# Performance work log

Hardware: AMD Instinct MI355X
Metric: run time of the kernel (lower is better)

## Reference

```python
import jax, jax.numpy as jnp
import numpy as np


def setup_inputs() -> dict:
    key = jax.random.key(0)
    ks = jax.random.split(key, 5)
    B, T, D, U = 32, 2048, 512, 512
    scale = 1.0 / np.sqrt(D)
    return {
        "full": jax.random.normal(ks[0], (B, T, D), jnp.float32),
        "last": jax.random.normal(ks[1], (B, D), jnp.float32),
        "W1": jax.random.normal(ks[2], (D, U), jnp.float32) * scale,
        "b1": jnp.zeros((U,), jnp.float32),
        "W2": jax.random.normal(ks[3], (D, U), jnp.float32) * scale,
        "b2": jnp.zeros((U,), jnp.float32),
        "V": jax.random.normal(ks[4], (U, 1), jnp.float32) * (1.0 / np.sqrt(U)),
        "bV": jnp.zeros((1,), jnp.float32),
    }


def reference(full, last, W1, b1, W2, b2, V, bV):
    # full: [B,T,D], last: [B,D]
    h1 = jnp.einsum("btd,du->btu", full, W1) + b1          # [B,T,U]
    h2 = last @ W2 + b2                                      # [B,U]
    score = jnp.tanh(h1 + h2[:, None, :]) @ V + bV           # [B,T,1]
    attn = jax.nn.softmax(score, axis=1)                     # [B,T,1]
    context = jnp.sum(attn * full, axis=1)                   # [B,D]
    return context
```

## Files before the change

### kernel.cpp

```cpp
#include <hip/hip_runtime.h>
#include <math.h>


#define BB 32
#define TT 2048
#define DD 512
#define UU 512

typedef short bf16x8 __attribute__((ext_vector_type(8)));
typedef short bf16x4 __attribute__((ext_vector_type(4)));
typedef float f32x4  __attribute__((ext_vector_type(4)));

static __device__ __forceinline__ short f2bf(float f) {
    unsigned x = __float_as_uint(f);
    return (short)((x + 0x7fffu + ((x >> 16) & 1u)) >> 16);
}

static __device__ __forceinline__ float fast_tanh(float x) {
    float e = __expf(2.f * x);
    return 1.f - 2.f * __builtin_amdgcn_rcpf(e + 1.f);
}

__global__ __launch_bounds__(256) void prep_kernel(const float* __restrict__ W1,
                                                   short* __restrict__ W1T,
                                                   const float* __restrict__ last,
                                                   const float* __restrict__ W2,
                                                   const float* __restrict__ b1,
                                                   const float* __restrict__ b2,
                                                   float* __restrict__ h2) {
    __shared__ float tile[32][33];
    __shared__ float ls[DD];
    const int bid = blockIdx.x;
    const int tid = threadIdx.x;
    if (bid < 256) {
        const int tr = (bid >> 4) << 5;
        const int tc = (bid & 15) << 5;
#pragma unroll
        for (int p = 0; p < 4; ++p) {
            const int r = p * 8 + (tid >> 5), c = tid & 31;
            tile[r][c] = W1[(size_t)(tr + r) * UU + tc + c];
        }
        __syncthreads();
#pragma unroll
        for (int p = 0; p < 4; ++p) {
            const int r = p * 8 + (tid >> 5), c = tid & 31;
            W1T[(size_t)(tc + r) * DD + tr + c] = f2bf(tile[c][r]);
        }
    } else {
        const int b = bid - 256;
        for (int i = tid; i < DD; i += 256) ls[i] = last[b * DD + i];
        __syncthreads();
        float a0 = 0.f, a1 = 0.f;
#pragma unroll 8
        for (int d = 0; d < DD; ++d) {
            const float l = ls[d];
            a0 += l * W2[d * UU + tid];
            a1 += l * W2[d * UU + tid + 256];
        }
        h2[b * UU + tid]       = a0 + b1[tid] + b2[tid];
        h2[b * UU + tid + 256] = a1 + b1[tid + 256] + b2[tid + 256];
    }
}

__global__ __launch_bounds__(256, 2) void score_kernel(const float* __restrict__ full,
                                                       const short* __restrict__ W1T,
                                                       const float* __restrict__ h2,
                                                       const float* __restrict__ V,
                                                       float* __restrict__ scores) {
    __shared__ __align__(16) short a_lds[64 * 40];
    __shared__ __align__(16) short b_lds[512 * 32];
    __shared__ float h2s[UU];
    __shared__ float Vs[UU];
    __shared__ float score_red[64];

    const int bid = blockIdx.x;
    const int b  = bid >> 5;
    const int t0 = (bid & 31) << 6;
    const int tid = threadIdx.x;
    const int w    = tid >> 6;
    const int lane = tid & 63;
    const int quad = lane >> 4;
    const int col  = lane & 15;

    for (int i = tid; i < UU; i += 256) { h2s[i] = h2[b * UU + i]; Vs[i] = V[i]; }
    if (tid < 64) score_red[tid] = 0.f;

    f32x4 acc[4][8];
#pragma unroll
    for (int i = 0; i < 4; ++i)
#pragma unroll
        for (int j = 0; j < 8; ++j) acc[i][j] = (f32x4){0.f, 0.f, 0.f, 0.f};

    const int arow = tid >> 3;
    const int ac   = (tid & 7) << 2;

    for (int k0 = 0; k0 < DD; k0 += 32) {
#pragma unroll
        for (int i = 0; i < 2; ++i) {
            const int row = arow + 32 * i;
            const float4 v = *(const float4*)&full[((size_t)(b * TT + t0 + row)) * DD + k0 + ac];
            bf16x4 s = {f2bf(v.x), f2bf(v.y), f2bf(v.z), f2bf(v.w)};
            *(bf16x4*)&a_lds[row * 40 + ac] = s;
        }
#pragma unroll
        for (int i = 0; i < 8; ++i) {
            const int id = (w * 8 + i) * 64 + lane;
            const int u  = id >> 2;
            const int c  = (id & 3) ^ (u & 3);
            const short* g = W1T + (size_t)u * DD + k0 + c * 8;
            __builtin_amdgcn_global_load_lds(
                (const __attribute__((address_space(1))) void*)g,
                (__attribute__((address_space(3))) void*)&b_lds[(w * 8 + i) * 64 * 8],
                16, 0, 0);
        }
        __syncthreads();

        bf16x8 af[4];
#pragma unroll
        for (int mt = 0; mt < 4; ++mt)
            af[mt] = *(const bf16x8*)&a_lds[(mt * 16 + col) * 40 + quad * 8];
#pragma unroll
        for (int nt = 0; nt < 8; ++nt) {
            const int u = w * 128 + nt * 16 + col;
            const bf16x8 bf = *(const bf16x8*)&b_lds[(u * 4 + (quad ^ (u & 3))) * 8];
#pragma unroll
            for (int mt = 0; mt < 4; ++mt)
                acc[mt][nt] = __builtin_amdgcn_mfma_f32_16x16x32_bf16(af[mt], bf, acc[mt][nt], 0, 0, 0);
        }
        __syncthreads();
    }

    float srow[16];
#pragma unroll
    for (int i = 0; i < 16; ++i) srow[i] = 0.f;
#pragma unroll
    for (int mt = 0; mt < 4; ++mt) {
#pragma unroll
        for (int nt = 0; nt < 8; ++nt) {
            const int u = w * 128 + nt * 16 + col;
            const float hv = h2s[u];
            const float vv = Vs[u];
#pragma unroll
            for (int r = 0; r < 4; ++r)
                srow[mt * 4 + r] += fast_tanh(acc[mt][nt][r] + hv) * vv;
        }
    }
#pragma unroll
    for (int off = 1; off < 16; off <<= 1) {
#pragma unroll
        for (int i = 0; i < 16; ++i) srow[i] += __shfl_xor(srow[i], off, 64);
    }
    if (col == 0) {
#pragma unroll
        for (int mt = 0; mt < 4; ++mt)
#pragma unroll
            for (int r = 0; r < 4; ++r)
                atomicAdd(&score_red[mt * 16 + quad * 4 + r], srow[mt * 4 + r]);
    }
    __syncthreads();
    if (tid < 64) scores[b * TT + t0 + tid] = score_red[tid];
}

__global__ __launch_bounds__(256) void softmax_kernel(float* __restrict__ scores,
                                                      float* __restrict__ out) {
    const int b = blockIdx.x;
    const int tid = threadIdx.x;
    __shared__ float red[256];

    out[b * DD + tid] = 0.f;
    out[b * DD + 256 + tid] = 0.f;

    float local[8];
    float m = -1e30f;
#pragma unroll
    for (int i = 0; i < 8; ++i) {
        local[i] = scores[b * TT + i * 256 + tid];
        m = fmaxf(m, local[i]);
    }
    red[tid] = m;
    __syncthreads();
    for (int s = 128; s > 0; s >>= 1) {
        if (tid < s) red[tid] = fmaxf(red[tid], red[tid + s]);
        __syncthreads();
    }
    const float mx = red[0];
    __syncthreads();

    float sum = 0.f;
#pragma unroll
    for (int i = 0; i < 8; ++i) {
        local[i] = __expf(local[i] - mx);
        sum += local[i];
    }
    red[tid] = sum;
    __syncthreads();
    for (int s = 128; s > 0; s >>= 1) {
        if (tid < s) red[tid] += red[tid + s];
        __syncthreads();
    }
    const float inv = 1.f / red[0];
#pragma unroll
    for (int i = 0; i < 8; ++i) scores[b * TT + i * 256 + tid] = local[i] * inv;
}

__global__ __launch_bounds__(256) void context_kernel(const float* __restrict__ full,
                                                      const float* __restrict__ p,
                                                      float* __restrict__ out) {
    const int bid = blockIdx.x;
    const int b  = bid >> 5;
    const int t0 = (bid & 31) << 6;
    const int tid = threadIdx.x;
    const int q   = tid & 127;
    const int par = tid >> 7;
    __shared__ float ps[64];
    __shared__ float4 red[128];
    if (tid < 64) ps[tid] = p[b * TT + t0 + tid];
    __syncthreads();

    float ax = 0.f, ay = 0.f, az = 0.f, aw = 0.f;
    const float* base = full + ((size_t)(b * TT + t0)) * DD;
#pragma unroll 4
    for (int it = 0; it < 32; ++it) {
        const int tl = it * 2 + par;
        const float4 v = *(const float4*)&base[(size_t)tl * DD + q * 4];
        const float wg = ps[tl];
        ax += wg * v.x; ay += wg * v.y; az += wg * v.z; aw += wg * v.w;
    }
    if (par == 1) red[q] = make_float4(ax, ay, az, aw);
    __syncthreads();
    if (par == 0) {
        const float4 o = red[q];
        atomicAdd(&out[b * DD + q * 4 + 0], ax + o.x);
        atomicAdd(&out[b * DD + q * 4 + 1], ay + o.y);
        atomicAdd(&out[b * DD + q * 4 + 2], az + o.z);
        atomicAdd(&out[b * DD + q * 4 + 3], aw + o.w);
    }
}

extern "C" void kernel_launch(void* const* d_in, const int* in_sizes, int n_in,
                              void* d_out, int out_size, void* d_ws, size_t ws_size,
                              hipStream_t stream) {
    const float* full = (const float*)d_in[0];
    const float* last = (const float*)d_in[1];
    const float* W1   = (const float*)d_in[2];
    const float* b1   = (const float*)d_in[3];
    const float* W2   = (const float*)d_in[4];
    const float* b2   = (const float*)d_in[5];
    const float* V    = (const float*)d_in[6];

    float* out    = (float*)d_out;
    float* scores = (float*)d_ws;
    float* h2     = (float*)d_ws + (size_t)BB * TT;
    short* W1T    = (short*)(h2 + (size_t)BB * UU);

    prep_kernel<<<256 + BB, 256, 0, stream>>>(W1, W1T, last, W2, b1, b2, h2);
    score_kernel<<<BB * (TT / 64), 256, 0, stream>>>(full, W1T, h2, V, scores);
    softmax_kernel<<<BB, 256, 0, stream>>>(scores, out);
    context_kernel<<<BB * (TT / 64), 256, 0, stream>>>(full, scores, out);
}
```

Baseline: 302.3 us.

## Load W1 fragments from global directly and restage A tiles with swizzled LDS

```diff
diff --git a/kernel.cpp b/kernel.cpp
--- a/kernel.cpp
+++ b/kernel.cpp
@@ -8,7 +8,6 @@
 #define UU 512
 
 typedef short bf16x8 __attribute__((ext_vector_type(8)));
-typedef short bf16x4 __attribute__((ext_vector_type(4)));
 typedef float f32x4  __attribute__((ext_vector_type(4)));
 
 static __device__ __forceinline__ short f2bf(float f) {
@@ -67,11 +66,8 @@
                                                        const float* __restrict__ h2,
                                                        const float* __restrict__ V,
                                                        float* __restrict__ scores) {
-    __shared__ __align__(16) short a_lds[64 * 40];
-    __shared__ __align__(16) short b_lds[512 * 32];
-    __shared__ float h2s[UU];
-    __shared__ float Vs[UU];
-    __shared__ float score_red[64];
+    __shared__ __align__(16) short a_lds[1024 * 8];
+    __shared__ float score_red[4][64];
 
     const int bid = blockIdx.x;
     const int b  = bid >> 5;
@@ -82,68 +78,63 @@
     const int quad = lane >> 4;
     const int col  = lane & 15;
 
-    for (int i = tid; i < UU; i += 256) { h2s[i] = h2[b * UU + i]; Vs[i] = V[i]; }
-    if (tid < 64) score_red[tid] = 0.f;
-
     f32x4 acc[4][8];
 #pragma unroll
     for (int i = 0; i < 4; ++i)
 #pragma unroll
         for (int j = 0; j < 8; ++j) acc[i][j] = (f32x4){0.f, 0.f, 0.f, 0.f};
 
-    const int arow = tid >> 3;
-    const int ac   = (tid & 7) << 2;
-
-    for (int k0 = 0; k0 < DD; k0 += 32) {
-#pragma unroll
-        for (int i = 0; i < 2; ++i) {
-            const int row = arow + 32 * i;
-            const float4 v = *(const float4*)&full[((size_t)(b * TT + t0 + row)) * DD + k0 + ac];
-            bf16x4 s = {f2bf(v.x), f2bf(v.y), f2bf(v.z), f2bf(v.w)};
-            *(bf16x4*)&a_lds[row * 40 + ac] = s;
-        }
-#pragma unroll
-        for (int i = 0; i < 8; ++i) {
-            const int id = (w * 8 + i) * 64 + lane;
-            const int u  = id >> 2;
-            const int c  = (id & 3) ^ (u & 3);
-            const short* g = W1T + (size_t)u * DD + k0 + c * 8;
-            __builtin_amdgcn_global_load_lds(
-                (const __attribute__((address_space(1))) void*)g,
-                (__attribute__((address_space(3))) void*)&b_lds[(w * 8 + i) * 64 * 8],
-                16, 0, 0);
-        }
-        __syncthreads();
-
-        bf16x8 af[4];
+    const size_t fullbase = (size_t)(b * TT + t0) * DD;
+    const short* bbase = W1T + (size_t)(w * 128 + col) * DD + quad * 8;
+
+    for (int ko = 0; ko < 4; ++ko) {
+        if (ko > 0) __syncthreads();
+#pragma unroll
+        for (int i = 0; i < 4; ++i) {
+            const int id  = tid + 256 * i;
+            const int row = id >> 4;
+            const int cc  = (id & 15) ^ (row & 15);
+            const float* src = &full[fullbase + (size_t)row * DD + ko * 128 + cc * 8];
+            const float4 v0 = *(const float4*)src;
+            const float4 v1 = *(const float4*)(src + 4);
+            bf16x8 pk = {f2bf(v0.x), f2bf(v0.y), f2bf(v0.z), f2bf(v0.w),
+                         f2bf(v1.x), f2bf(v1.y), f2bf(v1.z), f2bf(v1.w)};
+            *(bf16x8*)&a_lds[id * 8] = pk;
+        }
+        __syncthreads();
+
+        for (int ki = 0; ki < 4; ++ki) {
+            bf16x8 af[4];
+#pragma unroll
+            for (int mt = 0; mt < 4; ++mt) {
+                const int row = mt * 16 + col;
+                const int sl  = row * 16 + ((ki * 4 + quad) ^ col);
+                af[mt] = *(const bf16x8*)&a_lds[sl * 8];
+            }
+            const int kg = ko * 128 + ki * 32;
+#pragma unroll
+            for (int nt = 0; nt < 8; ++nt) {
+                const bf16x8 bf = *(const bf16x8*)&bbase[(size_t)nt * 16 * DD + kg];
+#pragma unroll
+                for (int mt = 0; mt < 4; ++mt)
+                    acc[mt][nt] = __builtin_amdgcn_mfma_f32_16x16x32_bf16(af[mt], bf, acc[mt][nt], 0, 0, 0);
+            }
+        }
+    }
+
+    float srow[16];
+#pragma unroll
+    for (int i = 0; i < 16; ++i) srow[i] = 0.f;
+#pragma unroll
+    for (int nt = 0; nt < 8; ++nt) {
+        const int u = w * 128 + nt * 16 + col;
+        const float hv = h2[b * UU + u];
+        const float vv = V[u];
 #pragma unroll
         for (int mt = 0; mt < 4; ++mt)
-            af[mt] = *(const bf16x8*)&a_lds[(mt * 16 + col) * 40 + quad * 8];
-#pragma unroll
-        for (int nt = 0; nt < 8; ++nt) {
-            const int u = w * 128 + nt * 16 + col;
-            const bf16x8 bf = *(const bf16x8*)&b_lds[(u * 4 + (quad ^ (u & 3))) * 8];
-#pragma unroll
-            for (int mt = 0; mt < 4; ++mt)
-                acc[mt][nt] = __builtin_amdgcn_mfma_f32_16x16x32_bf16(af[mt], bf, acc[mt][nt], 0, 0, 0);
-        }
-        __syncthreads();
-    }
-
-    float srow[16];
-#pragma unroll
-    for (int i = 0; i < 16; ++i) srow[i] = 0.f;
-#pragma unroll
-    for (int mt = 0; mt < 4; ++mt) {
-#pragma unroll
-        for (int nt = 0; nt < 8; ++nt) {
-            const int u = w * 128 + nt * 16 + col;
-            const float hv = h2s[u];
-            const float vv = Vs[u];
 #pragma unroll
             for (int r = 0; r < 4; ++r)
                 srow[mt * 4 + r] += fast_tanh(acc[mt][nt][r] + hv) * vv;
-        }
     }
 #pragma unroll
     for (int off = 1; off < 16; off <<= 1) {
@@ -155,10 +146,12 @@
         for (int mt = 0; mt < 4; ++mt)
 #pragma unroll
             for (int r = 0; r < 4; ++r)
-                atomicAdd(&score_red[mt * 16 + quad * 4 + r], srow[mt * 4 + r]);
-    }
-    __syncthreads();
-    if (tid < 64) scores[b * TT + t0 + tid] = score_red[tid];
+                score_red[w][mt * 16 + quad * 4 + r] = srow[mt * 4 + r];
+    }
+    __syncthreads();
+    if (tid < 64)
+        scores[b * TT + t0 + tid] = score_red[0][tid] + score_red[1][tid] +
+                                    score_red[2][tid] + score_red[3][tid];
 }
 
 __global__ __launch_bounds__(256) void softmax_kernel(float* __restrict__ scores,
@@ -207,33 +200,40 @@
                                                       const float* __restrict__ p,
                                                       float* __restrict__ out) {
     const int bid = blockIdx.x;
-    const int b  = bid >> 5;
-    const int t0 = (bid & 31) << 6;
-    const int tid = threadIdx.x;
-    const int q   = tid & 127;
-    const int par = tid >> 7;
-    __shared__ float ps[64];
-    __shared__ float4 red[128];
-    if (tid < 64) ps[tid] = p[b * TT + t0 + tid];
+    const int b  = bid >> 3;
+    const int d0 = ((bid >> 1) & 3) * 128;
+    const int t0 = (bid & 1) * 1024;
+    const int tid = threadIdx.x;
+    const int c  = tid & 31;
+    const int tr = tid >> 5;
+
+    __shared__ float ps[1024];
+    __shared__ float4 red[256];
+    for (int i = tid; i < 1024; i += 256) ps[i] = p[b * TT + t0 + i];
     __syncthreads();
 
     float ax = 0.f, ay = 0.f, az = 0.f, aw = 0.f;
-    const float* base = full + ((size_t)(b * TT + t0)) * DD;
+    const float* base = full + ((size_t)(b * TT + t0)) * DD + d0;
 #pragma unroll 4
-    for (int it = 0; it < 32; ++it) {
-        const int tl = it * 2 + par;
-        const float4 v = *(const float4*)&base[(size_t)tl * DD + q * 4];
-        const float wg = ps[tl];
+    for (int it = 0; it < 128; ++it) {
+        const int t = it * 8 + tr;
+        const float4 v = *(const float4*)&base[(size_t)t * DD + c * 4];
+        const float wg = ps[t];
         ax += wg * v.x; ay += wg * v.y; az += wg * v.z; aw += wg * v.w;
     }
-    if (par == 1) red[q] = make_float4(ax, ay, az, aw);
-    __syncthreads();
-    if (par == 0) {
-        const float4 o = red[q];
-        atomicAdd(&out[b * DD + q * 4 + 0], ax + o.x);
-        atomicAdd(&out[b * DD + q * 4 + 1], ay + o.y);
-        atomicAdd(&out[b * DD + q * 4 + 2], az + o.z);
-        atomicAdd(&out[b * DD + q * 4 + 3], aw + o.w);
+    red[tid] = make_float4(ax, ay, az, aw);
+    __syncthreads();
+    if (tid < 32) {
+        float4 s = red[tid];
+#pragma unroll
+        for (int g = 1; g < 8; ++g) {
+            const float4 o = red[g * 32 + tid];
+            s.x += o.x; s.y += o.y; s.z += o.z; s.w += o.w;
+        }
+        atomicAdd(&out[b * DD + d0 + tid * 4 + 0], s.x);
+        atomicAdd(&out[b * DD + d0 + tid * 4 + 1], s.y);
+        atomicAdd(&out[b * DD + d0 + tid * 4 + 2], s.z);
+        atomicAdd(&out[b * DD + d0 + tid * 4 + 3], s.w);
     }
 }
 
@@ -256,5 +256,5 @@
     prep_kernel<<<256 + BB, 256, 0, stream>>>(W1, W1T, last, W2, b1, b2, h2);
     score_kernel<<<BB * (TT / 64), 256, 0, stream>>>(full, W1T, h2, V, scores);
     softmax_kernel<<<BB, 256, 0, stream>>>(scores, out);
-    context_kernel<<<BB * (TT / 64), 256, 0, stream>>>(full, scores, out);
-}
+    context_kernel<<<256, 256, 0, stream>>>(full, scores, out);
+}
```

After: 314.9 us. 4.2% more time.
